# Optimization experiments

Measured on AMD Instinct MI355X. Metric: run time of the kernel, lower is better.

The kernel has to match this reference:

```python
import jax, jax.numpy as jnp
import numpy as np

B, H, W, C = 4, 128, 128, 256
D_MODEL, NH = 512, 8
DH = D_MODEL // NH  # 64


def setup_inputs() -> dict:
    key = jax.random.key(0)
    ks = jax.random.split(key, 5)
    s = lambda fan_in: 1.0 / np.sqrt(fan_in)
    return {
        "x": jax.random.normal(ks[0], (B, H, W, C), jnp.float32),
        "Wq": jax.random.normal(ks[1], (C, D_MODEL), jnp.float32) * s(C),
        "bq": jnp.zeros((D_MODEL,), jnp.float32),
        "Wk": jax.random.normal(ks[2], (C, D_MODEL), jnp.float32) * s(C),
        "bk": jnp.zeros((D_MODEL,), jnp.float32),
        "Wv": jax.random.normal(ks[3], (C, D_MODEL), jnp.float32) * s(C),
        "bv": jnp.zeros((D_MODEL,), jnp.float32),
        "Wo": jax.random.normal(ks[4], (D_MODEL, C), jnp.float32) * s(D_MODEL),
        "bo": jnp.zeros((C,), jnp.float32),
    }


def reference(x, Wq, bq, Wk, bk, Wv, bv, Wo, bo):
    # Axial multi-head attention along axis 1 (H), W axis is batched.
    b, h, w, _ = x.shape
    q = (x @ Wq + bq).reshape(b, h, w, NH, DH) * (DH ** -0.5)
    k = (x @ Wk + bk).reshape(b, h, w, NH, DH)
    v = (x @ Wv + bv).reshape(b, h, w, NH, DH)
    # scores over the H axis: [B, Nh, W, H, H]
    scores = jnp.einsum("bxwnd,bywnd->bnwxy", q, k)
    probs = jax.nn.softmax(scores, axis=-1)
    # [B, H, W, Nh, DH] -> [B, H, W, d_model]
    out = jnp.einsum("bnwxy,bywnd->bxwnd", probs, v).reshape(b, h, w, D_MODEL)
    # Wo projection; original combines to [B,W,H,C] then permutes back to [B,H,W,C],
    # which is equivalent to applying Wo directly here. Dropout is identity at inference.
    return out @ Wo + bo
```

## Files before the change

kernel.cpp:

```cpp
#include <hip/hip_runtime.h>

typedef unsigned short u16;
typedef __attribute__((ext_vector_type(8))) short bf16x8;
typedef __attribute__((ext_vector_type(8))) unsigned short u16x8;
typedef __attribute__((ext_vector_type(4))) unsigned u32x4;
typedef __attribute__((ext_vector_type(4))) float f32x4;

#define DEVI static __device__ __forceinline__

DEVI u16 f2b(float f) {
  unsigned u = __builtin_bit_cast(unsigned, f);
  return (u16)((u + 0x7FFFu + ((u >> 16) & 1u)) >> 16);
}

DEVI unsigned cvtpk(float a, float b) {
  unsigned r;
  asm("v_cvt_pk_bf16_f32 %0, %1, %2" : "=v"(r) : "v"(a), "v"(b));
  return r;
}

DEVI void gload_lds16(const void* g, void* l) {
  __builtin_amdgcn_global_load_lds(
      (const __attribute__((address_space(1))) unsigned int*)g,
      (__attribute__((address_space(3))) unsigned int*)l, 16, 0, 0);
}


__global__ __launch_bounds__(256) void prep_x(const float* __restrict__ x, u16* __restrict__ xb) {
  const int n8 = 65536 * 256 / 8;
  int i = blockIdx.x * blockDim.x + threadIdx.x;
  for (; i < n8; i += gridDim.x * blockDim.x) {
    const float4* p = (const float4*)x + (size_t)i * 2;
    float4 a = p[0], b = p[1];
    u16x8 r;
    r[0] = f2b(a.x); r[1] = f2b(a.y); r[2] = f2b(a.z); r[3] = f2b(a.w);
    r[4] = f2b(b.x); r[5] = f2b(b.y); r[6] = f2b(b.z); r[7] = f2b(b.w);
    *(u16x8*)(xb + (size_t)i * 8) = r;
  }
}

__global__ __launch_bounds__(256) void prep_w(
    const float* __restrict__ Wq, const float* __restrict__ Wk,
    const float* __restrict__ Wv, const float* __restrict__ Wo,
    const float* __restrict__ bq, const float* __restrict__ bk, const float* __restrict__ bv,
    u16* __restrict__ wqkvT, u16* __restrict__ woT, float* __restrict__ bqkv) {
  const int NW1 = 1536 * 256, NW2 = 256 * 512;
  const int total = NW1 + NW2 + 1536;
  int i = blockIdx.x * blockDim.x + threadIdx.x;
  for (; i < total; i += gridDim.x * blockDim.x) {
    if (i < NW1) {
      int nn = i >> 8, kk = i & 255;
      float v;
      if (nn < 512)       v = Wq[kk * 512 + nn] * 0.125f;
      else if (nn < 1024) v = Wk[kk * 512 + (nn - 512)];
      else                v = Wv[kk * 512 + (nn - 1024)];
      wqkvT[i] = f2b(v);
    } else if (i < NW1 + NW2) {
      int j = i - NW1;
      int nn = j >> 9, kk = j & 511;
      woT[j] = f2b(Wo[kk * 256 + nn]);
    } else {
      int j = i - NW1 - NW2;
      bqkv[j] = (j < 512) ? bq[j] * 0.125f : (j < 1024 ? bk[j - 512] : bv[j - 1024]);
    }
  }
}


template <int KK, bool OUT_BF16>
__global__ __launch_bounds__(1024) void gemm256(
    const u16* __restrict__ A, const u16* __restrict__ Bt,
    const float* __restrict__ bias, void* __restrict__ Cv, int N) {
  constexpr int NT = KK / 64;
  __shared__ u16 smem[65536];
  const int tid = threadIdx.x;
  const int lane = tid & 63, wid = tid >> 6;
  const int nTn = N >> 8;
  const int qx = gridDim.x >> 3;
  const int wg = (blockIdx.x & 7) * qx + (blockIdx.x >> 3);
  const long m0 = (long)(wg / nTn) * 256;
  const long n0 = (long)(wg % nTn) * 256;
  const int wr = wid >> 2, wc = wid & 3;
  const int hi = lane >> 4, lo = lane & 15;
  const u16* Ab = A + m0 * KK;
  const u16* Bb = Bt + n0 * KK;
  const int srow_ = tid >> 3;
  const int schunk = tid & 7;

  f32x4 acc[4][4];
#pragma unroll
  for (int mi = 0; mi < 4; ++mi)
#pragma unroll
    for (int ni = 0; ni < 4; ++ni) acc[mi][ni] = f32x4{0.f, 0.f, 0.f, 0.f};

  auto stage = [&](int t) {
    u16* base = &smem[(t & 1) * 32768];
    const int kt = t * 64;
#pragma unroll
    for (int j = 0; j < 2; ++j) {
      int row = j * 128 + srow_;
      int colE = (schunk ^ (row & 7)) << 3;
      gload_lds16(Ab + (long)row * KK + kt + colE, &base[(j * 1024 + tid) * 8]);
    }
#pragma unroll
    for (int j = 0; j < 2; ++j) {
      int row = j * 128 + srow_;
      int colE = (schunk ^ (row & 7)) << 3;
      gload_lds16(Bb + (long)row * KK + kt + colE, &base[16384 + (j * 1024 + tid) * 8]);
    }
  };

  stage(0);
#pragma unroll
  for (int t = 0; t < NT; ++t) {
    if (t + 1 < NT) {
      stage(t + 1);
      asm volatile("s_waitcnt vmcnt(4)" ::: "memory");
    } else {
      asm volatile("s_waitcnt vmcnt(0)" ::: "memory");
    }
    __builtin_amdgcn_sched_barrier(0);
    __builtin_amdgcn_s_barrier();
    const u16* aB = &smem[(t & 1) * 32768];
    const u16* bB = aB + 16384;
#pragma unroll
    for (int ks = 0; ks < 2; ++ks) {
      const int slot = ((hi + ks * 4) ^ (lo & 7)) << 3;
      bf16x8 af[4], bfr[4];
#pragma unroll
      for (int mi = 0; mi < 4; ++mi)
        af[mi] = *(const bf16x8*)&aB[(wr * 64 + mi * 16 + lo) * 64 + slot];
#pragma unroll
      for (int ni = 0; ni < 4; ++ni)
        bfr[ni] = *(const bf16x8*)&bB[(wc * 64 + ni * 16 + lo) * 64 + slot];
#pragma unroll
      for (int mi = 0; mi < 4; ++mi)
#pragma unroll
        for (int ni = 0; ni < 4; ++ni)
          acc[mi][ni] = __builtin_amdgcn_mfma_f32_16x16x32_bf16(af[mi], bfr[ni], acc[mi][ni], 0, 0, 0);
    }
    __builtin_amdgcn_sched_barrier(0);
    __builtin_amdgcn_s_barrier();
  }

  float bb[4];
#pragma unroll
  for (int ni = 0; ni < 4; ++ni) bb[ni] = bias[n0 + wc * 64 + ni * 16 + lo];

  if (OUT_BF16) {
    u16* Cg = (u16*)Cv;
#pragma unroll
    for (int mi = 0; mi < 4; ++mi)
#pragma unroll
      for (int ni = 0; ni < 4; ++ni) {
#pragma unroll
        for (int j = 0; j < 4; ++j) {
          int row = wr * 64 + mi * 16 + hi * 4 + j;
          int chunk = (wc * 8 + ni * 2 + (lo >> 3)) ^ ((row >> 2) & 7);
          smem[row * 256 + chunk * 8 + (lo & 7)] = f2b(acc[mi][ni][j] + bb[ni]);
        }
      }
    __syncthreads();
#pragma unroll
    for (int it = 0; it < 8; ++it) {
      int idx = it * 1024 + tid;
      int row = idx >> 5, c = idx & 31;
      int cs = c ^ ((row >> 2) & 7);
      *(u16x8*)(Cg + (m0 + row) * N + n0 + c * 8) = *(const u16x8*)&smem[row * 256 + cs * 8];
    }
  } else {
    float* Cg = (float*)Cv;
#pragma unroll
    for (int mi = 0; mi < 4; ++mi)
#pragma unroll
      for (int ni = 0; ni < 4; ++ni) {
        long cg = n0 + wc * 64 + ni * 16 + lo;
#pragma unroll
        for (int j = 0; j < 4; ++j)
          Cg[(m0 + wr * 64 + mi * 16 + hi * 4 + j) * N + cg] = acc[mi][ni][j] + bb[ni];
      }
  }
}


__global__ __launch_bounds__(256, 4) void attn_axial(const u16* __restrict__ qkv,
                                                     u16* __restrict__ ao) {
  __shared__ u16 smem[16384];
  u16* kld = smem;
  u16* vt  = smem + 8192;

  const int g = blockIdx.x;
  const int n = g & 7, w = (g >> 3) & 127, b = g >> 10;
  const int tid = threadIdx.x, lane = tid & 63, wid = tid >> 6;
  const size_t ystr = (size_t)128 * 1536;
  const size_t base = (size_t)(b * 16384 + w) * 1536;
  const size_t bq_ = base + n * 64;
  const size_t bk_ = base + 512 + n * 64;
  const size_t bv_ = base + 1024 + n * 64;
  const int hi = lane >> 4, lo = lane & 15;

  {
    const int kr0 = tid >> 3, kc = tid & 7;
#pragma unroll
    for (int i = 0; i < 4; ++i) {
      const int row = i * 32 + kr0;
      const int srcC = (kc ^ (row & 7)) << 3;
      gload_lds16(qkv + bk_ + (size_t)row * ystr + srcC, &kld[(i * 256 + tid) * 8]);
    }
  }

  const int vyp = (tid & 63) * 2;
  const u16* vg = qkv + bv_ + (size_t)vyp * ystr + wid * 16;
  u16x8 va0 = *(const u16x8*)vg;
  u16x8 va1 = *(const u16x8*)(vg + 8);
  u16x8 vc0 = *(const u16x8*)(vg + ystr);
  u16x8 vc1 = *(const u16x8*)(vg + ystr + 8);

  bf16x8 qf[2][2];
#pragma unroll
  for (int cg = 0; cg < 2; ++cg)
#pragma unroll
    for (int ks = 0; ks < 2; ++ks)
      qf[cg][ks] = *(const bf16x8*)(qkv + bq_ +
          (size_t)(wid * 32 + cg * 16 + lo) * ystr + hi * 8 + ks * 32);

  {
    unsigned* vt32 = (unsigned*)vt;
    const int cch = vyp >> 3;
    const int cw = (vyp >> 1) & 3;
#pragma unroll
    for (int e = 0; e < 8; ++e) {
      const int d0 = wid * 16 + e, d1 = wid * 16 + 8 + e;
      const int c0s = (cch & 8) | ((cch & 7) ^ (d0 & 7));
      const int c1s = (cch & 8) | ((cch & 7) ^ (d1 & 7));
      vt32[d0 * 64 + c0s * 4 + cw] = (unsigned)va0[e] | ((unsigned)vc0[e] << 16);
      vt32[d1 * 64 + c1s * 4 + cw] = (unsigned)va1[e] | ((unsigned)vc1[e] << 16);
    }
  }

  __syncthreads();

  f32x4 s2[2][8];
#pragma unroll
  for (int cg = 0; cg < 2; ++cg)
#pragma unroll
    for (int ni = 0; ni < 8; ++ni) s2[cg][ni] = f32x4{0.f, 0.f, 0.f, 0.f};
  __builtin_amdgcn_s_setprio(1);
#pragma unroll
  for (int ks = 0; ks < 2; ++ks)
#pragma unroll
    for (int ni = 0; ni < 8; ++ni) {
      const int kr = ni * 16 + lo;
      bf16x8 kf = *(const bf16x8*)&kld[kr * 64 + (((hi + ks * 4) ^ (kr & 7)) << 3)];
      s2[0][ni] = __builtin_amdgcn_mfma_f32_16x16x32_bf16(kf, qf[0][ks], s2[0][ni], 0, 0, 0);
      s2[1][ni] = __builtin_amdgcn_mfma_f32_16x16x32_bf16(kf, qf[1][ks], s2[1][ni], 0, 0, 0);
    }
  __builtin_amdgcn_s_setprio(0);

  unsigned setA[2][4][2], setB[2][4][2];
#pragma unroll
  for (int cg = 0; cg < 2; ++cg) {
    float mx = s2[cg][0][0];
#pragma unroll
    for (int ni = 0; ni < 8; ++ni)
#pragma unroll
      for (int j = 0; j < 4; ++j) mx = fmaxf(mx, s2[cg][ni][j]);
    mx = fmaxf(mx, __shfl_xor(mx, 16, 64));
    mx = fmaxf(mx, __shfl_xor(mx, 32, 64));
    float sum = 0.f;
#pragma unroll
    for (int ni = 0; ni < 8; ++ni)
#pragma unroll
      for (int j = 0; j < 4; ++j) {
        float e = exp2f((s2[cg][ni][j] - mx) * 1.44269504f);
        s2[cg][ni][j] = e;
        sum += e;
      }
    sum += __shfl_xor(sum, 16, 64);
    sum += __shfl_xor(sum, 32, 64);
    const float r = 1.f / sum;

    unsigned pkE[4][2], pkO[4][2];
#pragma unroll
    for (int o = 0; o < 4; ++o) {
      pkE[o][0] = cvtpk(s2[cg][2 * o][0] * r, s2[cg][2 * o][1] * r);
      pkE[o][1] = cvtpk(s2[cg][2 * o][2] * r, s2[cg][2 * o][3] * r);
      pkO[o][0] = cvtpk(s2[cg][2 * o + 1][0] * r, s2[cg][2 * o + 1][1] * r);
      pkO[o][1] = cvtpk(s2[cg][2 * o + 1][2] * r, s2[cg][2 * o + 1][3] * r);
    }
    const bool lowHi = (hi < 2);
    unsigned keepR[4][2], gotR[4][2];
#pragma unroll
    for (int o = 0; o < 4; ++o)
#pragma unroll
      for (int e = 0; e < 2; ++e) {
        unsigned snd = lowHi ? pkO[o][e] : pkE[o][e];
        keepR[o][e] = lowHi ? pkE[o][e] : pkO[o][e];
        gotR[o][e] = __shfl_xor(snd, 32, 64);
      }
    const bool fwdGot = (hi == 0) || (hi == 3);
    unsigned recv2[4][2];
#pragma unroll
    for (int o = 0; o < 4; ++o)
#pragma unroll
      for (int e = 0; e < 2; ++e) {
        unsigned snd = fwdGot ? gotR[o][e] : keepR[o][e];
        recv2[o][e] = __shfl_xor(snd, 16, 64);
      }
#pragma unroll
    for (int o = 0; o < 4; ++o)
#pragma unroll
      for (int e = 0; e < 2; ++e) {
        setA[cg][o][e] = (hi & 1) ? recv2[o][e] : (hi == 0 ? keepR[o][e] : gotR[o][e]);
        setB[cg][o][e] = (hi & 1) ? (hi == 1 ? gotR[o][e] : keepR[o][e]) : recv2[o][e];
      }
  }

  f32x4 o2[2][4];
#pragma unroll
  for (int cg = 0; cg < 2; ++cg)
#pragma unroll
    for (int ni = 0; ni < 4; ++ni) o2[cg][ni] = f32x4{0.f, 0.f, 0.f, 0.f};
  __builtin_amdgcn_s_setprio(1);
#pragma unroll
  for (int ks = 0; ks < 4; ++ks) {
    const int cch = hi + ks * 4;
    bf16x8 pa[2];
#pragma unroll
    for (int cg = 0; cg < 2; ++cg) {
      u32x4 t;
      t[0] = setA[cg][ks][0]; t[1] = setA[cg][ks][1];
      t[2] = setB[cg][ks][0]; t[3] = setB[cg][ks][1];
      pa[cg] = __builtin_bit_cast(bf16x8, t);
    }
#pragma unroll
    for (int ni = 0; ni < 4; ++ni) {
      const int vr = ni * 16 + lo;
      const int cs = (cch & 8) | ((cch & 7) ^ (vr & 7));
      bf16x8 vf = *(const bf16x8*)&vt[vr * 128 + cs * 8];
      o2[0][ni] = __builtin_amdgcn_mfma_f32_16x16x32_bf16(pa[0], vf, o2[0][ni], 0, 0, 0);
      o2[1][ni] = __builtin_amdgcn_mfma_f32_16x16x32_bf16(pa[1], vf, o2[1][ni], 0, 0, 0);
    }
  }
  __builtin_amdgcn_s_setprio(0);

#pragma unroll
  for (int cg = 0; cg < 2; ++cg)
#pragma unroll
    for (int j = 0; j < 4; ++j) {
      const int q = wid * 32 + cg * 16 + hi * 4 + j;
      const size_t obase = ((size_t)(b * 16384 + q * 128 + w)) * 512 + (size_t)n * 64;
#pragma unroll
      for (int ni = 0; ni < 4; ++ni)
        ao[obase + ni * 16 + lo] = f2b(o2[cg][ni][j]);
    }
}


extern "C" void kernel_launch(void* const* d_in, const int* in_sizes, int n_in,
                              void* d_out, int out_size, void* d_ws, size_t ws_size,
                              hipStream_t stream) {
  (void)in_sizes; (void)n_in; (void)out_size; (void)ws_size;
  const float* x  = (const float*)d_in[0];
  const float* Wq = (const float*)d_in[1];
  const float* bq = (const float*)d_in[2];
  const float* Wk = (const float*)d_in[3];
  const float* bk = (const float*)d_in[4];
  const float* Wv = (const float*)d_in[5];
  const float* bv = (const float*)d_in[6];
  const float* Wo = (const float*)d_in[7];
  const float* bo = (const float*)d_in[8];
  float* out = (float*)d_out;

  char* ws = (char*)d_ws;
  const size_t MiB = (size_t)1 << 20;
  u16* qkv   = (u16*)ws;
  u16* xb    = (u16*)(ws + 192 * MiB);
  u16* wqkvT = (u16*)(ws + 224 * MiB);
  u16* woT   = wqkvT + 1536 * 256;
  float* bqkv = (float*)(woT + 256 * 512);

  prep_x<<<2048, 256, 0, stream>>>(x, xb);
  prep_w<<<512, 256, 0, stream>>>(Wq, Wk, Wv, Wo, bq, bk, bv, wqkvT, woT, bqkv);

  gemm256<256, true><<<1536, 1024, 0, stream>>>(xb, wqkvT, bqkv, qkv, 1536);
  attn_axial<<<4096, 256, 0, stream>>>(qkv, (u16*)out);
  gemm256<512, false><<<256, 1024, 0, stream>>>((const u16*)out, woT, bo, out, 256);
}
```

Baseline: 225.3 us.

## Write QKV in per-(b,w,head) contiguous layout for axial attention

The QKV GEMM epilogue now scatters its bf16 output into a [B,W,head,{q,k,v},H,64] layout, so each attention block reads contiguous 16 KB Q, K and V tiles instead of rows strided by 128*1536 elements. This is meant to make the attention kernel's global loads fully coalesced and TLB/cache friendly, at the cost of a more scattered 16-byte store pattern in the GEMM epilogue. The attention kernel's launch bounds are also raised to request 5 blocks per CU.

New measurement: 210.4 us. 1.07x faster.

```diff
diff --git a/kernel.cpp b/kernel.cpp
--- a/kernel.cpp
+++ b/kernel.cpp
@@ -67,7 +67,7 @@
 }
 
 
-template <int KK, bool OUT_BF16>
+template <int KK, int OMODE>
 __global__ __launch_bounds__(1024) void gemm256(
     const u16* __restrict__ A, const u16* __restrict__ Bt,
     const float* __restrict__ bias, void* __restrict__ Cv, int N) {
@@ -147,7 +147,7 @@
 #pragma unroll
   for (int ni = 0; ni < 4; ++ni) bb[ni] = bias[n0 + wc * 64 + ni * 16 + lo];
 
-  if (OUT_BF16) {
+  if (OMODE == 2) {
     u16* Cg = (u16*)Cv;
 #pragma unroll
     for (int mi = 0; mi < 4; ++mi)
@@ -166,7 +166,13 @@
       int idx = it * 1024 + tid;
       int row = idx >> 5, c = idx & 31;
       int cs = c ^ ((row >> 2) & 7);
-      *(u16x8*)(Cg + (m0 + row) * N + n0 + c * 8) = *(const u16x8*)&smem[row * 256 + cs * 8];
+      long m = m0 + row;
+      int col = (int)n0 + c * 8;
+      int b_ = (int)(m >> 14), yw = (int)m & 16383;
+      int y = yw >> 7, w = yw & 127;
+      int t = col >> 9, h = (col >> 6) & 7, dh = col & 63;
+      size_t dst = ((((size_t)(b_ * 128 + w) * 8 + h) * 3 + t) * 128 + y) * 64 + dh;
+      *(u16x8*)(Cg + dst) = *(const u16x8*)&smem[row * 256 + cs * 8];
     }
   } else {
     float* Cg = (float*)Cv;
@@ -183,7 +189,7 @@
 }
 
 
-__global__ __launch_bounds__(256, 4) void attn_axial(const u16* __restrict__ qkv,
+__global__ __launch_bounds__(256, 5) void attn_axial(const u16* __restrict__ qkv,
                                                      u16* __restrict__ ao) {
   __shared__ u16 smem[16384];
   u16* kld = smem;
@@ -192,11 +198,10 @@
   const int g = blockIdx.x;
   const int n = g & 7, w = (g >> 3) & 127, b = g >> 10;
   const int tid = threadIdx.x, lane = tid & 63, wid = tid >> 6;
-  const size_t ystr = (size_t)128 * 1536;
-  const size_t base = (size_t)(b * 16384 + w) * 1536;
-  const size_t bq_ = base + n * 64;
-  const size_t bk_ = base + 512 + n * 64;
-  const size_t bv_ = base + 1024 + n * 64;
+  const size_t pq = (((size_t)(b * 128 + w) * 8 + n) * 3) * 8192;
+  const u16* Qp = qkv + pq;
+  const u16* Kp = qkv + pq + 8192;
+  const u16* Vp = qkv + pq + 16384;
   const int hi = lane >> 4, lo = lane & 15;
 
   {
@@ -205,24 +210,23 @@
     for (int i = 0; i < 4; ++i) {
       const int row = i * 32 + kr0;
       const int srcC = (kc ^ (row & 7)) << 3;
-      gload_lds16(qkv + bk_ + (size_t)row * ystr + srcC, &kld[(i * 256 + tid) * 8]);
+      gload_lds16(Kp + row * 64 + srcC, &kld[(i * 256 + tid) * 8]);
     }
   }
 
   const int vyp = (tid & 63) * 2;
-  const u16* vg = qkv + bv_ + (size_t)vyp * ystr + wid * 16;
+  const u16* vg = Vp + vyp * 64 + wid * 16;
   u16x8 va0 = *(const u16x8*)vg;
   u16x8 va1 = *(const u16x8*)(vg + 8);
-  u16x8 vc0 = *(const u16x8*)(vg + ystr);
-  u16x8 vc1 = *(const u16x8*)(vg + ystr + 8);
+  u16x8 vc0 = *(const u16x8*)(vg + 64);
+  u16x8 vc1 = *(const u16x8*)(vg + 72);
 
   bf16x8 qf[2][2];
 #pragma unroll
   for (int cg = 0; cg < 2; ++cg)
 #pragma unroll
     for (int ks = 0; ks < 2; ++ks)
-      qf[cg][ks] = *(const bf16x8*)(qkv + bq_ +
-          (size_t)(wid * 32 + cg * 16 + lo) * ystr + hi * 8 + ks * 32);
+      qf[cg][ks] = *(const bf16x8*)(Qp + (wid * 32 + cg * 16 + lo) * 64 + hi * 8 + ks * 32);
 
   {
     unsigned* vt32 = (unsigned*)vt;
@@ -383,7 +387,7 @@
   prep_x<<<2048, 256, 0, stream>>>(x, xb);
   prep_w<<<512, 256, 0, stream>>>(Wq, Wk, Wv, Wo, bq, bk, bv, wqkvT, woT, bqkv);
 
-  gemm256<256, true><<<1536, 1024, 0, stream>>>(xb, wqkvT, bqkv, qkv, 1536);
+  gemm256<256, 2><<<1536, 1024, 0, stream>>>(xb, wqkvT, bqkv, qkv, 1536);
   attn_axial<<<4096, 256, 0, stream>>>(qkv, (u16*)out);
-  gemm256<512, false><<<256, 1024, 0, stream>>>((const u16*)out, woT, bo, out, 256);
-}
+  gemm256<512, 0><<<256, 1024, 0, stream>>>((const u16*)out, woT, bo, out, 256);
+}
```

## Fuse QKV projection into axial attention kernel per head and column

Applied to the files above, without the earlier changes.

Replaces the separate QKV GEMM and attention kernels with one kernel that projects Q, K and V for a (batch, column, head) tile directly into LDS before running attention. x is re-laid out as [B,W,H,C] so each block reads contiguous rows. This removes the large bf16 qkv intermediate round trip through global memory. In exchange, each x tile is read once per head, weights are loaded from global per block, and register pressure rises from holding the whole x tile in VGPRs.

After: 223.2 us. No clear change (-0.9%).

```diff
diff --git a/kernel.cpp b/kernel.cpp
--- a/kernel.cpp
+++ b/kernel.cpp
@@ -3,6 +3,7 @@
 typedef unsigned short u16;
 typedef __attribute__((ext_vector_type(8))) short bf16x8;
 typedef __attribute__((ext_vector_type(8))) unsigned short u16x8;
+typedef __attribute__((ext_vector_type(4))) unsigned short u16x4;
 typedef __attribute__((ext_vector_type(4))) unsigned u32x4;
 typedef __attribute__((ext_vector_type(4))) float f32x4;
 
@@ -19,14 +20,8 @@
   return r;
 }
 
-DEVI void gload_lds16(const void* g, void* l) {
-  __builtin_amdgcn_global_load_lds(
-      (const __attribute__((address_space(1))) unsigned int*)g,
-      (__attribute__((address_space(3))) unsigned int*)l, 16, 0, 0);
-}
-
-
-__global__ __launch_bounds__(256) void prep_x(const float* __restrict__ x, u16* __restrict__ xb) {
+
+__global__ __launch_bounds__(256) void prep_x2(const float* __restrict__ x, u16* __restrict__ xb2) {
   const int n8 = 65536 * 256 / 8;
   int i = blockIdx.x * blockDim.x + threadIdx.x;
   for (; i < n8; i += gridDim.x * blockDim.x) {
@@ -35,7 +30,9 @@
     u16x8 r;
     r[0] = f2b(a.x); r[1] = f2b(a.y); r[2] = f2b(a.z); r[3] = f2b(a.w);
     r[4] = f2b(b.x); r[5] = f2b(b.y); r[6] = f2b(b.z); r[7] = f2b(b.w);
-    *(u16x8*)(xb + (size_t)i * 8) = r;
+    const int t = i >> 5, c0 = (i & 31) * 8;
+    const int b_ = t >> 14, y = (t >> 7) & 127, w = t & 127;
+    *(u16x8*)(xb2 + (((size_t)(b_ * 128 + w) * 128) + y) * 256 + c0) = r;
   }
 }
 
@@ -67,7 +64,266 @@
 }
 
 
-template <int KK, bool OUT_BF16>
+__global__ __launch_bounds__(256) void qkv_attn(
+    const u16* __restrict__ xb2, const u16* __restrict__ wqkvT,
+    const float* __restrict__ bqkv, u16* __restrict__ ao) {
+  __shared__ u16 smem[24576];
+  u16* qld = smem;
+  u16* kld = smem + 8192;
+  u16* vt  = smem + 16384;
+
+  const int g = blockIdx.x;
+  const int n = g & 7, ct = g >> 3;
+  const int tid = threadIdx.x, lane = tid & 63, wid = tid >> 6;
+  const int hi = lane >> 4, lo = lane & 15;
+  const int wr = wid >> 1, wc = wid & 1;
+
+  const u16* Xp = xb2 + (size_t)ct * 32768;
+  const u16* Wq = wqkvT + (size_t)(n * 64 + wc * 32) * 256;
+  const u16* Wk = Wq + 512 * 256;
+  const u16* Wv = Wq + 1024 * 256;
+
+  bf16x8 areg[4][8];
+#pragma unroll
+  for (int yT = 0; yT < 4; ++yT)
+#pragma unroll
+    for (int ks = 0; ks < 8; ++ks)
+      areg[yT][ks] = *(const bf16x8*)(Xp + (wr * 64 + yT * 16 + lo) * 256 + hi * 8 + ks * 32);
+
+  {
+    f32x4 acc[2][4];
+#pragma unroll
+    for (int dhT = 0; dhT < 2; ++dhT)
+#pragma unroll
+      for (int yT = 0; yT < 4; ++yT) acc[dhT][yT] = f32x4{0.f, 0.f, 0.f, 0.f};
+#pragma unroll
+    for (int ks = 0; ks < 8; ++ks) {
+      bf16x8 wf0 = *(const bf16x8*)(Wq + (0 * 16 + lo) * 256 + hi * 8 + ks * 32);
+      bf16x8 wf1 = *(const bf16x8*)(Wq + (1 * 16 + lo) * 256 + hi * 8 + ks * 32);
+#pragma unroll
+      for (int yT = 0; yT < 4; ++yT) {
+        acc[0][yT] = __builtin_amdgcn_mfma_f32_16x16x32_bf16(wf0, areg[yT][ks], acc[0][yT], 0, 0, 0);
+        acc[1][yT] = __builtin_amdgcn_mfma_f32_16x16x32_bf16(wf1, areg[yT][ks], acc[1][yT], 0, 0, 0);
+      }
+    }
+#pragma unroll
+    for (int dhT = 0; dhT < 2; ++dhT) {
+      const int dh0 = wc * 32 + dhT * 16 + hi * 4;
+      float4 bq4 = *(const float4*)&bqkv[n * 64 + dh0];
+#pragma unroll
+      for (int yT = 0; yT < 4; ++yT) {
+        const int y = wr * 64 + yT * 16 + lo;
+        u16x4 pk;
+        pk[0] = f2b(acc[dhT][yT][0] + bq4.x);
+        pk[1] = f2b(acc[dhT][yT][1] + bq4.y);
+        pk[2] = f2b(acc[dhT][yT][2] + bq4.z);
+        pk[3] = f2b(acc[dhT][yT][3] + bq4.w);
+        *(u16x4*)&qld[y * 64 + (((dh0 >> 3) ^ (y & 7)) << 3) + (dh0 & 7)] = pk;
+      }
+    }
+  }
+
+  {
+    f32x4 acc[2][4];
+#pragma unroll
+    for (int dhT = 0; dhT < 2; ++dhT)
+#pragma unroll
+      for (int yT = 0; yT < 4; ++yT) acc[dhT][yT] = f32x4{0.f, 0.f, 0.f, 0.f};
+#pragma unroll
+    for (int ks = 0; ks < 8; ++ks) {
+      bf16x8 wf0 = *(const bf16x8*)(Wk + (0 * 16 + lo) * 256 + hi * 8 + ks * 32);
+      bf16x8 wf1 = *(const bf16x8*)(Wk + (1 * 16 + lo) * 256 + hi * 8 + ks * 32);
+#pragma unroll
+      for (int yT = 0; yT < 4; ++yT) {
+        acc[0][yT] = __builtin_amdgcn_mfma_f32_16x16x32_bf16(wf0, areg[yT][ks], acc[0][yT], 0, 0, 0);
+        acc[1][yT] = __builtin_amdgcn_mfma_f32_16x16x32_bf16(wf1, areg[yT][ks], acc[1][yT], 0, 0, 0);
+      }
+    }
+#pragma unroll
+    for (int dhT = 0; dhT < 2; ++dhT) {
+      const int dh0 = wc * 32 + dhT * 16 + hi * 4;
+#pragma unroll
+      for (int yT = 0; yT < 4; ++yT) {
+        const int y = wr * 64 + yT * 16 + lo;
+        u16x4 pk;
+        pk[0] = f2b(acc[dhT][yT][0]);
+        pk[1] = f2b(acc[dhT][yT][1]);
+        pk[2] = f2b(acc[dhT][yT][2]);
+        pk[3] = f2b(acc[dhT][yT][3]);
+        *(u16x4*)&kld[y * 64 + (((dh0 >> 3) ^ (y & 7)) << 3) + (dh0 & 7)] = pk;
+      }
+    }
+  }
+
+  {
+    f32x4 acc[4][2];
+#pragma unroll
+    for (int yT = 0; yT < 4; ++yT)
+#pragma unroll
+      for (int dhT = 0; dhT < 2; ++dhT) acc[yT][dhT] = f32x4{0.f, 0.f, 0.f, 0.f};
+#pragma unroll
+    for (int ks = 0; ks < 8; ++ks) {
+      bf16x8 wf0 = *(const bf16x8*)(Wv + (0 * 16 + lo) * 256 + hi * 8 + ks * 32);
+      bf16x8 wf1 = *(const bf16x8*)(Wv + (1 * 16 + lo) * 256 + hi * 8 + ks * 32);
+#pragma unroll
+      for (int yT = 0; yT < 4; ++yT) {
+        acc[yT][0] = __builtin_amdgcn_mfma_f32_16x16x32_bf16(areg[yT][ks], wf0, acc[yT][0], 0, 0, 0);
+        acc[yT][1] = __builtin_amdgcn_mfma_f32_16x16x32_bf16(areg[yT][ks], wf1, acc[yT][1], 0, 0, 0);
+      }
+    }
+#pragma unroll
+    for (int dhT = 0; dhT < 2; ++dhT) {
+      const int dh = wc * 32 + dhT * 16 + lo;
+      const float bv = bqkv[1024 + n * 64 + dh];
+#pragma unroll
+      for (int yT = 0; yT < 4; ++yT) {
+        const int y0 = wr * 64 + yT * 16 + hi * 4;
+        const int cch = y0 >> 3;
+        u16x4 pk;
+        pk[0] = f2b(acc[yT][dhT][0] + bv);
+        pk[1] = f2b(acc[yT][dhT][1] + bv);
+        pk[2] = f2b(acc[yT][dhT][2] + bv);
+        pk[3] = f2b(acc[yT][dhT][3] + bv);
+        *(u16x4*)&vt[dh * 128 + (((cch & 8) | ((cch & 7) ^ (dh & 7))) << 3) + (y0 & 7)] = pk;
+      }
+    }
+  }
+
+  __syncthreads();
+
+  bf16x8 qf[2][2];
+#pragma unroll
+  for (int cg = 0; cg < 2; ++cg)
+#pragma unroll
+    for (int ks = 0; ks < 2; ++ks) {
+      const int qr = wid * 32 + cg * 16 + lo;
+      qf[cg][ks] = *(const bf16x8*)&qld[qr * 64 + (((hi + ks * 4) ^ (qr & 7)) << 3)];
+    }
+  f32x4 s2[2][8];
+#pragma unroll
+  for (int cg = 0; cg < 2; ++cg)
+#pragma unroll
+    for (int ni = 0; ni < 8; ++ni) s2[cg][ni] = f32x4{0.f, 0.f, 0.f, 0.f};
+  __builtin_amdgcn_s_setprio(1);
+#pragma unroll
+  for (int ks = 0; ks < 2; ++ks)
+#pragma unroll
+    for (int ni = 0; ni < 8; ++ni) {
+      const int kr = ni * 16 + lo;
+      bf16x8 kf = *(const bf16x8*)&kld[kr * 64 + (((hi + ks * 4) ^ (kr & 7)) << 3)];
+      s2[0][ni] = __builtin_amdgcn_mfma_f32_16x16x32_bf16(kf, qf[0][ks], s2[0][ni], 0, 0, 0);
+      s2[1][ni] = __builtin_amdgcn_mfma_f32_16x16x32_bf16(kf, qf[1][ks], s2[1][ni], 0, 0, 0);
+    }
+  __builtin_amdgcn_s_setprio(0);
+
+  unsigned setA[2][4][2], setB[2][4][2];
+#pragma unroll
+  for (int cg = 0; cg < 2; ++cg) {
+    float mx = s2[cg][0][0];
+#pragma unroll
+    for (int ni = 0; ni < 8; ++ni)
+#pragma unroll
+      for (int j = 0; j < 4; ++j) mx = fmaxf(mx, s2[cg][ni][j]);
+    mx = fmaxf(mx, __shfl_xor(mx, 16, 64));
+    mx = fmaxf(mx, __shfl_xor(mx, 32, 64));
+    float sum = 0.f;
+#pragma unroll
+    for (int ni = 0; ni < 8; ++ni)
+#pragma unroll
+      for (int j = 0; j < 4; ++j) {
+        float e = exp2f((s2[cg][ni][j] - mx) * 1.44269504f);
+        s2[cg][ni][j] = e;
+        sum += e;
+      }
+    sum += __shfl_xor(sum, 16, 64);
+    sum += __shfl_xor(sum, 32, 64);
+    const float r = 1.f / sum;
+
+    unsigned pkE[4][2], pkO[4][2];
+#pragma unroll
+    for (int o = 0; o < 4; ++o) {
+      pkE[o][0] = cvtpk(s2[cg][2 * o][0] * r, s2[cg][2 * o][1] * r);
+      pkE[o][1] = cvtpk(s2[cg][2 * o][2] * r, s2[cg][2 * o][3] * r);
+      pkO[o][0] = cvtpk(s2[cg][2 * o + 1][0] * r, s2[cg][2 * o + 1][1] * r);
+      pkO[o][1] = cvtpk(s2[cg][2 * o + 1][2] * r, s2[cg][2 * o + 1][3] * r);
+    }
+    const bool lowHi = (hi < 2);
+    unsigned keepR[4][2], gotR[4][2];
+#pragma unroll
+    for (int o = 0; o < 4; ++o)
+#pragma unroll
+      for (int e = 0; e < 2; ++e) {
+        unsigned snd = lowHi ? pkO[o][e] : pkE[o][e];
+        keepR[o][e] = lowHi ? pkE[o][e] : pkO[o][e];
+        gotR[o][e] = __shfl_xor(snd, 32, 64);
+      }
+    const bool fwdGot = (hi == 0) || (hi == 3);
+    unsigned recv2[4][2];
+#pragma unroll
+    for (int o = 0; o < 4; ++o)
+#pragma unroll
+      for (int e = 0; e < 2; ++e) {
+        unsigned snd = fwdGot ? gotR[o][e] : keepR[o][e];
+        recv2[o][e] = __shfl_xor(snd, 16, 64);
+      }
+#pragma unroll
+    for (int o = 0; o < 4; ++o)
+#pragma unroll
+      for (int e = 0; e < 2; ++e) {
+        setA[cg][o][e] = (hi & 1) ? recv2[o][e] : (hi == 0 ? keepR[o][e] : gotR[o][e]);
+        setB[cg][o][e] = (hi & 1) ? (hi == 1 ? gotR[o][e] : keepR[o][e]) : recv2[o][e];
+      }
+  }
+
+  f32x4 o2[2][4];
+#pragma unroll
+  for (int cg = 0; cg < 2; ++cg)
+#pragma unroll
+    for (int ni = 0; ni < 4; ++ni) o2[cg][ni] = f32x4{0.f, 0.f, 0.f, 0.f};
+  __builtin_amdgcn_s_setprio(1);
+#pragma unroll
+  for (int ks = 0; ks < 4; ++ks) {
+    const int cch = hi + ks * 4;
+    bf16x8 pa[2];
+#pragma unroll
+    for (int cg = 0; cg < 2; ++cg) {
+      u32x4 t;
+      t[0] = setA[cg][ks][0]; t[1] = setA[cg][ks][1];
+      t[2] = setB[cg][ks][0]; t[3] = setB[cg][ks][1];
+      pa[cg] = __builtin_bit_cast(bf16x8, t);
+    }
+#pragma unroll
+    for (int ni = 0; ni < 4; ++ni) {
+      const int vr = ni * 16 + lo;
+      const int cs = (cch & 8) | ((cch & 7) ^ (vr & 7));
+      bf16x8 vf = *(const bf16x8*)&vt[vr * 128 + cs * 8];
+      o2[0][ni] = __builtin_amdgcn_mfma_f32_16x16x32_bf16(pa[0], vf, o2[0][ni], 0, 0, 0);
+      o2[1][ni] = __builtin_amdgcn_mfma_f32_16x16x32_bf16(pa[1], vf, o2[1][ni], 0, 0, 0);
+    }
+  }
+  __builtin_amdgcn_s_setprio(0);
+
+  const int b_ = ct >> 7, w_ = ct & 127;
+#pragma unroll
+  for (int cg = 0; cg < 2; ++cg)
+#pragma unroll
+    for (int j = 0; j < 4; ++j) {
+      const int q = wid * 32 + cg * 16 + hi * 4 + j;
+      const size_t obase = ((size_t)(b_ * 16384 + q * 128 + w_)) * 512 + (size_t)n * 64;
+#pragma unroll
+      for (int ni = 0; ni < 4; ++ni)
+        ao[obase + ni * 16 + lo] = f2b(o2[cg][ni][j]);
+    }
+}
+
+
+DEVI void gload_lds16(const void* g, void* l) {
+  __builtin_amdgcn_global_load_lds(
+      (const __attribute__((address_space(1))) unsigned int*)g,
+      (__attribute__((address_space(3))) unsigned int*)l, 16, 0, 0);
+}
+
+template <int KK>
 __global__ __launch_bounds__(1024) void gemm256(
     const u16* __restrict__ A, const u16* __restrict__ Bt,
     const float* __restrict__ bias, void* __restrict__ Cv, int N) {
@@ -147,212 +403,15 @@
 #pragma unroll
   for (int ni = 0; ni < 4; ++ni) bb[ni] = bias[n0 + wc * 64 + ni * 16 + lo];
 
-  if (OUT_BF16) {
-    u16* Cg = (u16*)Cv;
-#pragma unroll
-    for (int mi = 0; mi < 4; ++mi)
-#pragma unroll
-      for (int ni = 0; ni < 4; ++ni) {
-#pragma unroll
-        for (int j = 0; j < 4; ++j) {
-          int row = wr * 64 + mi * 16 + hi * 4 + j;
-          int chunk = (wc * 8 + ni * 2 + (lo >> 3)) ^ ((row >> 2) & 7);
-          smem[row * 256 + chunk * 8 + (lo & 7)] = f2b(acc[mi][ni][j] + bb[ni]);
-        }
-      }
-    __syncthreads();
-#pragma unroll
-    for (int it = 0; it < 8; ++it) {
-      int idx = it * 1024 + tid;
-      int row = idx >> 5, c = idx & 31;
-      int cs = c ^ ((row >> 2) & 7);
-      *(u16x8*)(Cg + (m0 + row) * N + n0 + c * 8) = *(const u16x8*)&smem[row * 256 + cs * 8];
-    }
-  } else {
-    float* Cg = (float*)Cv;
-#pragma unroll
-    for (int mi = 0; mi < 4; ++mi)
-#pragma unroll
-      for (int ni = 0; ni < 4; ++ni) {
-        long cg = n0 + wc * 64 + ni * 16 + lo;
-#pragma unroll
-        for (int j = 0; j < 4; ++j)
-          Cg[(m0 + wr * 64 + mi * 16 + hi * 4 + j) * N + cg] = acc[mi][ni][j] + bb[ni];
-      }
-  }
-}
-
-
-__global__ __launch_bounds__(256, 4) void attn_axial(const u16* __restrict__ qkv,
-                                                     u16* __restrict__ ao) {
-  __shared__ u16 smem[16384];
-  u16* kld = smem;
-  u16* vt  = smem + 8192;
-
-  const int g = blockIdx.x;
-  const int n = g & 7, w = (g >> 3) & 127, b = g >> 10;
-  const int tid = threadIdx.x, lane = tid & 63, wid = tid >> 6;
-  const size_t ystr = (size_t)128 * 1536;
-  const size_t base = (size_t)(b * 16384 + w) * 1536;
-  const size_t bq_ = base + n * 64;
-  const size_t bk_ = base + 512 + n * 64;
-  const size_t bv_ = base + 1024 + n * 64;
-  const int hi = lane >> 4, lo = lane & 15;
-
-  {
-    const int kr0 = tid >> 3, kc = tid & 7;
-#pragma unroll
-    for (int i = 0; i < 4; ++i) {
-      const int row = i * 32 + kr0;
-      const int srcC = (kc ^ (row & 7)) << 3;
-      gload_lds16(qkv + bk_ + (size_t)row * ystr + srcC, &kld[(i * 256 + tid) * 8]);
-    }
-  }
-
-  const int vyp = (tid & 63) * 2;
-  const u16* vg = qkv + bv_ + (size_t)vyp * ystr + wid * 16;
-  u16x8 va0 = *(const u16x8*)vg;
-  u16x8 va1 = *(const u16x8*)(vg + 8);
-  u16x8 vc0 = *(const u16x8*)(vg + ystr);
-  u16x8 vc1 = *(const u16x8*)(vg + ystr + 8);
-
-  bf16x8 qf[2][2];
-#pragma unroll
-  for (int cg = 0; cg < 2; ++cg)
-#pragma unroll
-    for (int ks = 0; ks < 2; ++ks)
-      qf[cg][ks] = *(const bf16x8*)(qkv + bq_ +
-          (size_t)(wid * 32 + cg * 16 + lo) * ystr + hi * 8 + ks * 32);
-
-  {
-    unsigned* vt32 = (unsigned*)vt;
-    const int cch = vyp >> 3;
-    const int cw = (vyp >> 1) & 3;
-#pragma unroll
-    for (int e = 0; e < 8; ++e) {
-      const int d0 = wid * 16 + e, d1 = wid * 16 + 8 + e;
-      const int c0s = (cch & 8) | ((cch & 7) ^ (d0 & 7));
-      const int c1s = (cch & 8) | ((cch & 7) ^ (d1 & 7));
-      vt32[d0 * 64 + c0s * 4 + cw] = (unsigned)va0[e] | ((unsigned)vc0[e] << 16);
-      vt32[d1 * 64 + c1s * 4 + cw] = (unsigned)va1[e] | ((unsigned)vc1[e] << 16);
-    }
-  }
-
-  __syncthreads();
-
-  f32x4 s2[2][8];
-#pragma unroll
-  for (int cg = 0; cg < 2; ++cg)
-#pragma unroll
-    for (int ni = 0; ni < 8; ++ni) s2[cg][ni] = f32x4{0.f, 0.f, 0.f, 0.f};
-  __builtin_amdgcn_s_setprio(1);
-#pragma unroll
-  for (int ks = 0; ks < 2; ++ks)
-#pragma unroll
-    for (int ni = 0; ni < 8; ++ni) {
-      const int kr = ni * 16 + lo;
-      bf16x8 kf = *(const bf16x8*)&kld[kr * 64 + (((hi + ks * 4) ^ (kr & 7)) << 3)];
-      s2[0][ni] = __builtin_amdgcn_mfma_f32_16x16x32_bf16(kf, qf[0][ks], s2[0][ni], 0, 0, 0);
-      s2[1][ni] = __builtin_amdgcn_mfma_f32_16x16x32_bf16(kf, qf[1][ks], s2[1][ni], 0, 0, 0);
-    }
-  __builtin_amdgcn_s_setprio(0);
-
-  unsigned setA[2][4][2], setB[2][4][2];
-#pragma unroll
-  for (int cg = 0; cg < 2; ++cg) {
-    float mx = s2[cg][0][0];
-#pragma unroll
-    for (int ni = 0; ni < 8; ++ni)
-#pragma unroll
-      for (int j = 0; j < 4; ++j) mx = fmaxf(mx, s2[cg][ni][j]);
-    mx = fmaxf(mx, __shfl_xor(mx, 16, 64));
-    mx = fmaxf(mx, __shfl_xor(mx, 32, 64));
-    float sum = 0.f;
-#pragma unroll
-    for (int ni = 0; ni < 8; ++ni)
-#pragma unroll
-      for (int j = 0; j < 4; ++j) {
-        float e = exp2f((s2[cg][ni][j] - mx) * 1.44269504f);
-        s2[cg][ni][j] = e;
-        sum += e;
-      }
-    sum += __shfl_xor(sum, 16, 64);
-    sum += __shfl_xor(sum, 32, 64);
-    const float r = 1.f / sum;
-
-    unsigned pkE[4][2], pkO[4][2];
-#pragma unroll
-    for (int o = 0; o < 4; ++o) {
-      pkE[o][0] = cvtpk(s2[cg][2 * o][0] * r, s2[cg][2 * o][1] * r);
-      pkE[o][1] = cvtpk(s2[cg][2 * o][2] * r, s2[cg][2 * o][3] * r);
-      pkO[o][0] = cvtpk(s2[cg][2 * o + 1][0] * r, s2[cg][2 * o + 1][1] * r);
-      pkO[o][1] = cvtpk(s2[cg][2 * o + 1][2] * r, s2[cg][2 * o + 1][3] * r);
-    }
-    const bool lowHi = (hi < 2);
-    unsigned keepR[4][2], gotR[4][2];
-#pragma unroll
-    for (int o = 0; o < 4; ++o)
-#pragma unroll
-      for (int e = 0; e < 2; ++e) {
-        unsigned snd = lowHi ? pkO[o][e] : pkE[o][e];
-        keepR[o][e] = lowHi ? pkE[o][e] : pkO[o][e];
-        gotR[o][e] = __shfl_xor(snd, 32, 64);
-      }
-    const bool fwdGot = (hi == 0) || (hi == 3);
-    unsigned recv2[4][2];
-#pragma unroll
-    for (int o = 0; o < 4; ++o)
-#pragma unroll
-      for (int e = 0; e < 2; ++e) {
-        unsigned snd = fwdGot ? gotR[o][e] : keepR[o][e];
-        recv2[o][e] = __shfl_xor(snd, 16, 64);
-      }
-#pragma unroll
-    for (int o = 0; o < 4; ++o)
-#pragma unroll
-      for (int e = 0; e < 2; ++e) {
-        setA[cg][o][e] = (hi & 1) ? recv2[o][e] : (hi == 0 ? keepR[o][e] : gotR[o][e]);
-        setB[cg][o][e] = (hi & 1) ? (hi == 1 ? gotR[o][e] : keepR[o][e]) : recv2[o][e];
-      }
-  }
-
-  f32x4 o2[2][4];
-#pragma unroll
-  for (int cg = 0; cg < 2; ++cg)
-#pragma unroll
-    for (int ni = 0; ni < 4; ++ni) o2[cg][ni] = f32x4{0.f, 0.f, 0.f, 0.f};
-  __builtin_amdgcn_s_setprio(1);
-#pragma unroll
-  for (int ks = 0; ks < 4; ++ks) {
-    const int cch = hi + ks * 4;
-    bf16x8 pa[2];
-#pragma unroll
-    for (int cg = 0; cg < 2; ++cg) {
-      u32x4 t;
-      t[0] = setA[cg][ks][0]; t[1] = setA[cg][ks][1];
-      t[2] = setB[cg][ks][0]; t[3] = setB[cg][ks][1];
-      pa[cg] = __builtin_bit_cast(bf16x8, t);
-    }
+  float* Cg = (float*)Cv;
+#pragma unroll
+  for (int mi = 0; mi < 4; ++mi)
 #pragma unroll
     for (int ni = 0; ni < 4; ++ni) {
-      const int vr = ni * 16 + lo;
-      const int cs = (cch & 8) | ((cch & 7) ^ (vr & 7));
-      bf16x8 vf = *(const bf16x8*)&vt[vr * 128 + cs * 8];
-      o2[0][ni] = __builtin_amdgcn_mfma_f32_16x16x32_bf16(pa[0], vf, o2[0][ni], 0, 0, 0);
-      o2[1][ni] = __builtin_amdgcn_mfma_f32_16x16x32_bf16(pa[1], vf, o2[1][ni], 0, 0, 0);
-    }
-  }
-  __builtin_amdgcn_s_setprio(0);
-
-#pragma unroll
-  for (int cg = 0; cg < 2; ++cg)
-#pragma unroll
-    for (int j = 0; j < 4; ++j) {
-      const int q = wid * 32 + cg * 16 + hi * 4 + j;
-      const size_t obase = ((size_t)(b * 16384 + q * 128 + w)) * 512 + (size_t)n * 64;
-#pragma unroll
-      for (int ni = 0; ni < 4; ++ni)
-        ao[obase + ni * 16 + lo] = f2b(o2[cg][ni][j]);
+      long cg = n0 + wc * 64 + ni * 16 + lo;
+#pragma unroll
+      for (int j = 0; j < 4; ++j)
+        Cg[(m0 + wr * 64 + mi * 16 + hi * 4 + j) * N + cg] = acc[mi][ni][j] + bb[ni];
     }
 }
 
@@ -374,16 +433,14 @@
 
   char* ws = (char*)d_ws;
   const size_t MiB = (size_t)1 << 20;
-  u16* qkv   = (u16*)ws;
-  u16* xb    = (u16*)(ws + 192 * MiB);
+  u16* xb2   = (u16*)(ws + 192 * MiB);
   u16* wqkvT = (u16*)(ws + 224 * MiB);
   u16* woT   = wqkvT + 1536 * 256;
   float* bqkv = (float*)(woT + 256 * 512);
 
-  prep_x<<<2048, 256, 0, stream>>>(x, xb);
+  prep_x2<<<2048, 256, 0, stream>>>(x, xb2);
   prep_w<<<512, 256, 0, stream>>>(Wq, Wk, Wv, Wo, bq, bk, bv, wqkvT, woT, bqkv);
 
-  gemm256<256, true><<<1536, 1024, 0, stream>>>(xb, wqkvT, bqkv, qkv, 1536);
-  attn_axial<<<4096, 256, 0, stream>>>(qkv, (u16*)out);
-  gemm256<512, false><<<256, 1024, 0, stream>>>((const u16*)out, woT, bo, out, 256);
-}
+  qkv_attn<<<4096, 256, 0, stream>>>(xb2, wqkvT, bqkv, (u16*)out);
+  gemm256<512><<<256, 1024, 0, stream>>>((const u16*)out, woT, bo, out, 256);
+}
```
